# Performance work log

Measured on AMD Instinct MI355X. Metric: run time of the kernel, lower is better.

## Reference

```python
import jax, jax.numpy as jnp
import numpy as np
import math

NUM_HEADS = 8


def setup_inputs() -> dict:
    key = jax.random.key(0)
    ks = jax.random.split(key, 6)
    b, s, e = 4, 2048, 512
    x = jax.random.normal(ks[0], (b, s, e), dtype=jnp.float32)
    # 0/1 adjacency matrix as float (it multiplies the scores in the module)
    adj = jax.random.randint(ks[1], (b, s, s), 0, 2).astype(jnp.float32)
    scale = 0.02
    Wqkv_w = jax.random.normal(ks[2], (3 * e, e), dtype=jnp.float32) * scale
    Wqkv_b = jax.random.normal(ks[3], (3 * e,), dtype=jnp.float32) * scale
    out_w = jax.random.normal(ks[4], (e, e), dtype=jnp.float32) * scale
    out_b = jax.random.normal(ks[5], (e,), dtype=jnp.float32) * scale
    return {"x": x, "adj": adj, "Wqkv_w": Wqkv_w, "Wqkv_b": Wqkv_b,
            "out_w": out_w, "out_b": out_b}


def reference(x, adj, Wqkv_w, Wqkv_b, out_w, out_b):
    b, s, e = x.shape
    h = NUM_HEADS
    d = e // h
    # fused qkv projection: (b, s, 3*e) -> (b, s, 3, h, d)
    qkv = (x @ Wqkv_w.T + Wqkv_b).reshape(b, s, 3, h, d)
    qkv = jnp.transpose(qkv, (2, 0, 3, 1, 4))  # (3, b, h, s, d)
    q, k, v = qkv[0], qkv[1], qkv[2]
    inv_sqrt_d = 1.0 / math.sqrt(d)
    scores = jnp.einsum('bhqd,bhkd->bhqk', q, k) * inv_sqrt_d
    scores = jnp.clip(scores * adj[:, None, :, :], -10000.0, 10000.0)
    attn = jax.nn.softmax(scores, axis=-1)
    out = jnp.einsum('bhqk,bhkd->bhqd', attn, v)
    out = jnp.transpose(out, (0, 2, 1, 3)).reshape(b, s, e)  # (b, s, h*d)
    return out @ out_w.T + out_b
```

## Files before the change

kernel.cpp:

```cpp
#include <hip/hip_runtime.h>


typedef __attribute__((ext_vector_type(8))) short bf16x8;
typedef __attribute__((ext_vector_type(4))) float f32x4;
typedef __attribute__((ext_vector_type(4))) unsigned short ushort4v;
typedef __attribute__((ext_vector_type(4))) _Float16 f16x4;
typedef __attribute__((ext_vector_type(8))) _Float16 f16x8;
typedef __attribute__((ext_vector_type(2))) __fp16 h16x2;
typedef __attribute__((ext_vector_type(2))) unsigned long long u64x2;

#if __has_builtin(__builtin_amdgcn_exp2f)
#define EXP2F(x) __builtin_amdgcn_exp2f(x)
#else
#define EXP2F(x) exp2f(x)
#endif

#define QSCALE 0.18033688011112042f

__device__ __forceinline__ unsigned short f2bf(float f) {
  unsigned int u = __float_as_uint(f);
  u += 0x7FFFu + ((u >> 16) & 1u);
  return (unsigned short)(u >> 16);
}
__device__ __forceinline__ unsigned short f2h(float f) {
  union { _Float16 h; unsigned short u; } cv;
  cv.h = (_Float16)f;
  return cv.u;
}

__device__ __forceinline__ int sbit(unsigned w, int pos) {
  return ((int)(w << (31 - pos))) >> 31;
}

__device__ __forceinline__ f16x8 pk8(const float* p) {
  union { struct { h16x2 a, b, c, d; } s; f16x8 v; } u;
  u.s.a = __builtin_amdgcn_cvt_pkrtz(p[0], p[1]);
  u.s.b = __builtin_amdgcn_cvt_pkrtz(p[2], p[3]);
  u.s.c = __builtin_amdgcn_cvt_pkrtz(p[4], p[5]);
  u.s.d = __builtin_amdgcn_cvt_pkrtz(p[6], p[7]);
  return u.v;
}

__device__ __forceinline__ f32x4 mfma_pv(f16x8 a, f16x8 b, f32x4 c) {
#if __has_builtin(__builtin_amdgcn_mfma_f32_16x16x32_f16)
  return __builtin_amdgcn_mfma_f32_16x16x32_f16(a, b, c, 0, 0, 0);
#else
  union { f16x8 v; struct { f16x4 lo, hi; } s; } ua, ub;
  ua.v = a; ub.v = b;
  c = __builtin_amdgcn_mfma_f32_16x16x16f16(ua.s.lo, ub.s.lo, c, 0, 0, 0);
  return __builtin_amdgcn_mfma_f32_16x16x16f16(ua.s.hi, ub.s.hi, c, 0, 0, 0);
#endif
}

__global__ __launch_bounds__(256) void prep_k(const float* __restrict__ x,
                                              unsigned short* __restrict__ x_bf,
                                              const float* __restrict__ wqkv,
                                              unsigned short* __restrict__ wqkv_bf,
                                              const float* __restrict__ outw,
                                              unsigned short* __restrict__ outw_bf,
                                              const float* __restrict__ adj,
                                              unsigned long long* __restrict__ abits) {
  const int bid = blockIdx.x;
  if (bid < 5120) {
    const float* in; unsigned short* out; int i;
    if (bid < 4096) { in = x; out = x_bf; i = bid * 256 + threadIdx.x; }
    else if (bid < 4864) { in = wqkv; out = wqkv_bf; i = (bid - 4096) * 256 + threadIdx.x; }
    else { in = outw; out = outw_bf; i = (bid - 4864) * 256 + threadIdx.x; }
    float4 v = ((const float4*)in)[i];
    ushort4v o;
    o[0] = f2bf(v.x); o[1] = f2bf(v.y); o[2] = f2bf(v.z); o[3] = f2bf(v.w);
    ((ushort4v*)out)[i] = o;
  } else {
    const int gw = (bid - 5120) * 4 + (threadIdx.x >> 6);
    const int l = threadIdx.x & 63;
    const int b = gw >> 11, q = gw & 2047;
    const float4* row = (const float4*)(adj + ((size_t)b * 2048 + q) * 2048) + l;
    unsigned long long* ob = abits + ((size_t)b * 8 * 2048 + q) * 4;
#pragma unroll
    for (int it = 0; it < 8; ++it) {
      const float4 v = row[(size_t)it * 64];
      const unsigned long long w0 = __ballot(v.x != 0.f);
      const unsigned long long w1 = __ballot(v.y != 0.f);
      const unsigned long long w2 = __ballot(v.z != 0.f);
      const unsigned long long w3 = __ballot(v.w != 0.f);
      if (l == 0) {
        ob[(size_t)it * 8192 + 0] = w0;
        ob[(size_t)it * 8192 + 1] = w1;
        ob[(size_t)it * 8192 + 2] = w2;
        ob[(size_t)it * 8192 + 3] = w3;
      }
    }
  }
}

__global__ __launch_bounds__(256, 3) void gemm128_k(const unsigned short* __restrict__ A,
                                                    const unsigned short* __restrict__ Bt,
                                                    const float* __restrict__ bias, int Kdim,
                                                    int Ntiles, unsigned short* __restrict__ q_out,
                                                    unsigned short* __restrict__ k_out,
                                                    unsigned short* __restrict__ v_out) {
  __shared__ union {
    struct { unsigned short A[2][128][40], B[2][128][40]; } s;
    unsigned short T[64][136];
  } u;

  const int t = threadIdx.x;
  const int lane = t & 63, w = t >> 6, ln = lane & 15, quad = lane >> 4;
  const int xcd = blockIdx.x & 7, loc = blockIdx.x >> 3;
  const int mt = xcd * ((gridDim.x >> 3) / Ntiles) + loc / Ntiles;
  const int nt = loc % Ntiles;
  const int wm = (w >> 1) * 64, wn = (w & 1) * 64;
  const int strow = t >> 2, stcol = (t & 3) * 8;

  const size_t abase = (size_t)(mt * 128 + strow) * Kdim + stcol;
  const size_t bbase = (size_t)(nt * 128 + strow) * Kdim + stcol;

  f32x4 acc[4][4];
#pragma unroll
  for (int i = 0; i < 4; ++i)
#pragma unroll
    for (int j = 0; j < 4; ++j) acc[i][j] = (f32x4){0.f, 0.f, 0.f, 0.f};

  bf16x8 a0 = *(const bf16x8*)(A + abase);
  bf16x8 a1 = *(const bf16x8*)(A + abase + (size_t)64 * Kdim);
  bf16x8 b0 = *(const bf16x8*)(Bt + bbase);
  bf16x8 b1 = *(const bf16x8*)(Bt + bbase + (size_t)64 * Kdim);
  *(bf16x8*)&u.s.A[0][strow][stcol] = a0;
  *(bf16x8*)&u.s.A[0][64 + strow][stcol] = a1;
  *(bf16x8*)&u.s.B[0][strow][stcol] = b0;
  *(bf16x8*)&u.s.B[0][64 + strow][stcol] = b1;
  __syncthreads();

  const int iters = Kdim >> 5;
  for (int it = 0; it < iters; ++it) {
    const int cur = it & 1, nxt = cur ^ 1;

    const int kn = ((it + 1) << 5) & (Kdim - 1);
    a0 = *(const bf16x8*)(A + abase + kn);
    a1 = *(const bf16x8*)(A + abase + (size_t)64 * Kdim + kn);
    b0 = *(const bf16x8*)(Bt + bbase + kn);
    b1 = *(const bf16x8*)(Bt + bbase + (size_t)64 * Kdim + kn);

    bf16x8 bfr[4];
#pragma unroll
    for (int nf = 0; nf < 4; ++nf)
      bfr[nf] = *(const bf16x8*)&u.s.B[cur][wn + nf * 16 + ln][quad * 8];
#pragma unroll
    for (int mf = 0; mf < 4; ++mf) {
      bf16x8 af = *(const bf16x8*)&u.s.A[cur][wm + mf * 16 + ln][quad * 8];
#pragma unroll
      for (int nf = 0; nf < 4; ++nf)
        acc[mf][nf] = __builtin_amdgcn_mfma_f32_16x16x32_bf16(af, bfr[nf], acc[mf][nf], 0, 0, 0);
    }

    if (it + 1 < iters) {
      *(bf16x8*)&u.s.A[nxt][strow][stcol] = a0;
      *(bf16x8*)&u.s.A[nxt][64 + strow][stcol] = a1;
      *(bf16x8*)&u.s.B[nxt][strow][stcol] = b0;
      *(bf16x8*)&u.s.B[nxt][64 + strow][stcol] = b1;
      __syncthreads();
    }
  }

  if (nt >= 8) {
    const int bb = mt >> 4, sq0 = (mt & 15) * 128;
#pragma unroll
    for (int half = 0; half < 2; ++half) {
      __syncthreads();
      if ((w & 1) == half) {
#pragma unroll
        for (int nf = 0; nf < 4; ++nf) {
          const float bv = bias[nt * 128 + half * 64 + nf * 16 + ln];
#pragma unroll
          for (int mf = 0; mf < 4; ++mf)
#pragma unroll
            for (int r = 0; r < 4; ++r)
              u.T[nf * 16 + ln][wm + mf * 16 + quad * 4 + r] = f2h(acc[mf][nf][r] + bv);
        }
      }
      __syncthreads();
#pragma unroll
      for (int rep = 0; rep < 4; ++rep) {
        const int row = rep * 16 + (t >> 4), c = t & 15;
        const bf16x8 val = *(const bf16x8*)&u.T[row][c * 8];
        const int hd = (nt - 8) * 128 + half * 64 + row;
        const int hh = hd >> 6, dd = hd & 63;
        *(bf16x8*)(v_out + ((size_t)(bb * 8 + hh) * 64 + dd) * 2048 + sq0 + c * 8) = val;
      }
    }
    return;
  }

#pragma unroll
  for (int mf = 0; mf < 4; ++mf) {
    const int m = mt * 128 + wm + mf * 16 + quad * 4;
#pragma unroll
    for (int nf = 0; nf < 4; ++nf) {
      const int n = nt * 128 + wn + nf * 16 + ln;
      const float bv = bias[n];
      const int hd = n & 511;
      const int hh = hd >> 6, dd = hd & 63;
      const int bb = m >> 11, sq = m & 2047;
      if (n < 512) {
#pragma unroll
        for (int r = 0; r < 4; ++r)
          q_out[((size_t)(bb * 8 + hh) * 2048 + sq + r) * 64 + dd] =
              f2bf((acc[mf][nf][r] + bv) * QSCALE);
      } else {
#pragma unroll
        for (int r = 0; r < 4; ++r)
          k_out[((size_t)(bb * 8 + hh) * 2048 + sq + r) * 64 + dd] = f2bf(acc[mf][nf][r] + bv);
      }
    }
  }
}

__global__ __launch_bounds__(256, 4) void gemm64_k(const unsigned short* __restrict__ A,
                                                   const unsigned short* __restrict__ Bt,
                                                   const float* __restrict__ bias,
                                                   float* __restrict__ f_out) {
  __shared__ struct { unsigned short A[2][64][40], B[2][64][40]; } s;

  const int t = threadIdx.x;
  const int lane = t & 63, w = t >> 6, ln = lane & 15, quad = lane >> 4;
  const int xcd = blockIdx.x & 7, loc = blockIdx.x >> 3;
  const int mt = xcd * 16 + (loc >> 3);
  const int nt = loc & 7;
  const int wm = (w >> 1) * 32, wn = (w & 1) * 32;
  const int strow = t >> 2, stcol = (t & 3) * 8;

  const size_t abase = (size_t)(mt * 64 + strow) * 512 + stcol;
  const size_t bbase = (size_t)(nt * 64 + strow) * 512 + stcol;

  f32x4 acc[2][2];
#pragma unroll
  for (int i = 0; i < 2; ++i)
#pragma unroll
    for (int j = 0; j < 2; ++j) acc[i][j] = (f32x4){0.f, 0.f, 0.f, 0.f};

  bf16x8 a0 = *(const bf16x8*)(A + abase);
  bf16x8 b0 = *(const bf16x8*)(Bt + bbase);
  *(bf16x8*)&s.A[0][strow][stcol] = a0;
  *(bf16x8*)&s.B[0][strow][stcol] = b0;
  __syncthreads();

  for (int it = 0; it < 16; ++it) {
    const int cur = it & 1, nxt = cur ^ 1;

    const int kn = ((it + 1) << 5) & 511;
    a0 = *(const bf16x8*)(A + abase + kn);
    b0 = *(const bf16x8*)(Bt + bbase + kn);

    bf16x8 bfr[2];
#pragma unroll
    for (int nf = 0; nf < 2; ++nf)
      bfr[nf] = *(const bf16x8*)&s.B[cur][wn + nf * 16 + ln][quad * 8];
#pragma unroll
    for (int mf = 0; mf < 2; ++mf) {
      bf16x8 af = *(const bf16x8*)&s.A[cur][wm + mf * 16 + ln][quad * 8];
#pragma unroll
      for (int nf = 0; nf < 2; ++nf)
        acc[mf][nf] = __builtin_amdgcn_mfma_f32_16x16x32_bf16(af, bfr[nf], acc[mf][nf], 0, 0, 0);
    }

    if (it + 1 < 16) {
      *(bf16x8*)&s.A[nxt][strow][stcol] = a0;
      *(bf16x8*)&s.B[nxt][strow][stcol] = b0;
      __syncthreads();
    }
  }

#pragma unroll
  for (int mf = 0; mf < 2; ++mf) {
    const int m = mt * 64 + wm + mf * 16 + quad * 4;
#pragma unroll
    for (int nf = 0; nf < 2; ++nf) {
      const int n = nt * 64 + wn + nf * 16 + ln;
      const float bv = bias[n];
#pragma unroll
      for (int r = 0; r < 4; ++r) f_out[(size_t)(m + r) * 512 + n] = acc[mf][nf][r] + bv;
    }
  }
}

__global__ __launch_bounds__(256, 2) void attn_k(const unsigned short* __restrict__ Qg,
                                                 const unsigned short* __restrict__ Kg,
                                                 const unsigned short* __restrict__ Vg,
                                                 const unsigned long long* __restrict__ Mg,
                                                 unsigned short* __restrict__ Og) {
  __shared__ unsigned short K_lds[2][64][64];
  __shared__ unsigned short V_lds[2][64][64];

  const int t = threadIdx.x;
  const int w = t >> 6, lane = t & 63, ln = lane & 15, quad = lane >> 4;
  const int bh = blockIdx.x & 31, qt = blockIdx.x >> 5, bb = bh >> 3;
  const int sbase = qt * 128;

  const unsigned short* Qp = Qg + (size_t)bh * (2048 * 64);
  const unsigned short* Kp = Kg + (size_t)bh * (2048 * 64);
  const unsigned short* Vp = Vg + (size_t)bh * (64 * 2048);
  const unsigned long long* Mb = Mg + ((size_t)bb * 8 * 2048 + sbase + w * 32 + ln) * 4;

  bf16x8 qf[2][2];
#pragma unroll
  for (int qg = 0; qg < 2; ++qg) {
    const int qrow = sbase + w * 32 + qg * 16 + ln;
    qf[qg][0] = *(const bf16x8*)(Qp + (size_t)qrow * 64 + quad * 8);
    qf[qg][1] = *(const bf16x8*)(Qp + (size_t)qrow * 64 + 32 + quad * 8);
  }

  const _Float16 one_h = (_Float16)((ln == 0) ? 1.0f : 0.0f);
  const f16x8 vf_one = (f16x8){one_h, one_h, one_h, one_h, one_h, one_h, one_h, one_h};

  const f32x4 zf = (f32x4){0.f, 0.f, 0.f, 0.f};

  f32x4 acc_o[2][4];
#pragma unroll
  for (int qg = 0; qg < 2; ++qg)
#pragma unroll
    for (int dg = 0; dg < 4; ++dg) acc_o[qg][dg] = zf;
  f32x4 acc_1[2] = {zf, zf};

  const int strow = t >> 2;
  const int stcol = (t & 3) * 16;
  const int c0 = (t & 3) * 2;
  const int gkw = (strow & 3) | (((strow >> 3) & 1) << 2);
  const int gvw = strow & 7;

  const unsigned short* Kl = Kp + (size_t)strow * 64 + stcol;
  const unsigned short* Vl = Vp + (size_t)strow * 2048 + stcol;

  bf16x8 kr0 = *(const bf16x8*)(Kl);
  bf16x8 kr1 = *(const bf16x8*)(Kl + 8);
  bf16x8 vr0 = *(const bf16x8*)(Vl);
  bf16x8 vr1 = *(const bf16x8*)(Vl + 8);
  *(bf16x8*)&K_lds[0][strow][(c0 ^ gkw) << 3] = kr0;
  *(bf16x8*)&K_lds[0][strow][((c0 + 1) ^ gkw) << 3] = kr1;
  *(bf16x8*)&V_lds[0][strow][(c0 ^ gvw) << 3] = vr0;
  *(bf16x8*)&V_lds[0][strow][((c0 + 1) ^ gvw) << 3] = vr1;
  u64x2 Wlo[2], Whi[2];
#pragma unroll
  for (int qg = 0; qg < 2; ++qg) {
    Wlo[qg] = *(const u64x2*)(Mb + qg * 64);
    Whi[qg] = *(const u64x2*)(Mb + qg * 64 + 2);
  }
  __syncthreads();

  const int kperm = ((ln >> 2) << 3) + (ln & 3);
  const int gkr = (ln & 3) | (((ln >> 2) & 1) << 2);
  const int gvr = ln & 7;
  const int kc = (quad ^ gkr) << 3;
  const unsigned q2 = quad << 1;

  for (int kts = 0; kts < 8; ++kts) {
    const size_t itn = (size_t)((kts < 7) ? kts + 1 : 0) * 8192;
    u64x2 nWlo[2], nWhi[2];
#pragma unroll
    for (int qg = 0; qg < 2; ++qg) {
      nWlo[qg] = *(const u64x2*)(Mb + itn + qg * 64);
      nWhi[qg] = *(const u64x2*)(Mb + itn + qg * 64 + 2);
    }

#pragma unroll
    for (int j = 0; j < 4; ++j) {
      const int kt = kts * 4 + j;
      const int cur = j & 1, nxt = cur ^ 1;

      kr0 = *(const bf16x8*)(Kl + (size_t)(kt + 1) * 4096);
      kr1 = *(const bf16x8*)(Kl + (size_t)(kt + 1) * 4096 + 8);
      vr0 = *(const bf16x8*)(Vl + (kt + 1) * 64);
      vr1 = *(const bf16x8*)(Vl + (kt + 1) * 64 + 8);

      f32x4 sc[2][4];
      __builtin_amdgcn_s_setprio(1);
#pragma unroll
      for (int h = 0; h < 2; ++h)
#pragma unroll
        for (int e = 0; e < 2; ++e) {
          const int krow = h * 32 + kperm + e * 4;
          bf16x8 kf0 = *(const bf16x8*)&K_lds[cur][krow][kc];
          bf16x8 kf1 = *(const bf16x8*)&K_lds[cur][krow][kc ^ 32];
#pragma unroll
          for (int qg = 0; qg < 2; ++qg) {
            f32x4 z = __builtin_amdgcn_mfma_f32_16x16x32_bf16(kf0, qf[qg][0], zf, 0, 0, 0);
            sc[qg][h * 2 + e] = __builtin_amdgcn_mfma_f32_16x16x32_bf16(kf1, qf[qg][1], z, 0, 0, 0);
          }
        }
      __builtin_amdgcn_s_setprio(0);

      f16x8 vfa[2][4];
#pragma unroll
      for (int h = 0; h < 2; ++h)
#pragma unroll
        for (int dg = 0; dg < 4; ++dg)
          vfa[h][dg] = *(const f16x8*)&V_lds[cur][dg * 16 + ln][((h * 4 + quad) ^ gvr) << 3];

      f16x8 pa[2][2];
#pragma unroll
      for (int qg = 0; qg < 2; ++qg) {
        const unsigned s0 = (unsigned)(Wlo[qg][0] >> (j >= 2 ? 32 : 0)) >> q2;
        const unsigned s1 = (unsigned)(Wlo[qg][1] >> (j >= 2 ? 32 : 0)) >> q2;
        const unsigned s2 = (unsigned)(Whi[qg][0] >> (j >= 2 ? 32 : 0)) >> q2;
        const unsigned s3 = (unsigned)(Whi[qg][1] >> (j >= 2 ? 32 : 0)) >> q2;
#pragma unroll
        for (int h = 0; h < 2; ++h) {
          float p[8];
#pragma unroll
          for (int e = 0; e < 2; ++e) {
            const int pos = (j & 1) * 16 + h * 8 + e;
            p[e * 4 + 0] =
                EXP2F(__int_as_float(__float_as_int(sc[qg][h * 2 + e][0]) & sbit(s0, pos)));
            p[e * 4 + 1] =
                EXP2F(__int_as_float(__float_as_int(sc[qg][h * 2 + e][1]) & sbit(s1, pos)));
            p[e * 4 + 2] =
                EXP2F(__int_as_float(__float_as_int(sc[qg][h * 2 + e][2]) & sbit(s2, pos)));
            p[e * 4 + 3] =
                EXP2F(__int_as_float(__float_as_int(sc[qg][h * 2 + e][3]) & sbit(s3, pos)));
          }
          pa[qg][h] = pk8(p);
        }
      }

      __builtin_amdgcn_s_setprio(1);
#pragma unroll
      for (int h = 0; h < 2; ++h)
#pragma unroll
        for (int qg = 0; qg < 2; ++qg) {
#pragma unroll
          for (int dg = 0; dg < 4; ++dg)
            acc_o[qg][dg] = mfma_pv(pa[qg][h], vfa[h][dg], acc_o[qg][dg]);
          acc_1[qg] = mfma_pv(pa[qg][h], vf_one, acc_1[qg]);
        }
      __builtin_amdgcn_s_setprio(0);

      if (kt < 31) {
        *(bf16x8*)&K_lds[nxt][strow][(c0 ^ gkw) << 3] = kr0;
        *(bf16x8*)&K_lds[nxt][strow][((c0 + 1) ^ gkw) << 3] = kr1;
        *(bf16x8*)&V_lds[nxt][strow][(c0 ^ gvw) << 3] = vr0;
        *(bf16x8*)&V_lds[nxt][strow][((c0 + 1) ^ gvw) << 3] = vr1;
        __syncthreads();
      }
    }
    Wlo[0] = nWlo[0]; Wlo[1] = nWlo[1];
    Whi[0] = nWhi[0]; Whi[1] = nWhi[1];
  }

  unsigned short* Op = Og + (size_t)bb * 2048 * 512 + (size_t)(bh & 7) * 64;
#pragma unroll
  for (int qg = 0; qg < 2; ++qg)
#pragma unroll
    for (int r = 0; r < 4; ++r) {
      const float inv = 1.0f / __shfl(acc_1[qg][r], quad * 16);
      const int sq = sbase + w * 32 + qg * 16 + quad * 4 + r;
#pragma unroll
      for (int dg = 0; dg < 4; ++dg)
        Op[(size_t)sq * 512 + dg * 16 + ln] = f2bf(acc_o[qg][dg][r] * inv);
    }
}

extern "C" void kernel_launch(void* const* d_in, const int* in_sizes, int n_in, void* d_out,
                              int out_size, void* d_ws, size_t ws_size, hipStream_t stream) {
  const float* x = (const float*)d_in[0];
  const float* adj = (const float*)d_in[1];
  const float* wqkv = (const float*)d_in[2];
  const float* bqkv = (const float*)d_in[3];
  const float* outw = (const float*)d_in[4];
  const float* outb = (const float*)d_in[5];
  float* out = (float*)d_out;

  char* ws = (char*)d_ws;
  unsigned short* x_bf = (unsigned short*)(ws);
  unsigned short* wqkv_bf = (unsigned short*)(ws + 8388608);
  unsigned short* outw_bf = (unsigned short*)(ws + 9961472);
  unsigned long long* abits = (unsigned long long*)(ws + 10485760);
  unsigned short* Qb = (unsigned short*)(ws + 27262976);
  unsigned short* Kb = (unsigned short*)(ws + 35651584);
  unsigned short* Vb = (unsigned short*)(ws + 44040192);
  unsigned short* Ob = (unsigned short*)(ws + 52428800);

  prep_k<<<7168, 256, 0, stream>>>(x, x_bf, wqkv, wqkv_bf, outw, outw_bf, adj, abits);

  gemm128_k<<<768, 256, 0, stream>>>(x_bf, wqkv_bf, bqkv, 512, 12, Qb, Kb, Vb);

  attn_k<<<512, 256, 0, stream>>>(Qb, Kb, Vb, abits, Ob);

  gemm64_k<<<1024, 256, 0, stream>>>(Ob, outw_bf, outb, out);
}
```

Before: 200.6 us.

## Fuse all stages into one persistent kernel with grid barriers

Merges the prep, QKV GEMM, attention and output GEMM kernels into a single persistent launch of 512 blocks that loops over the former block indices, with atomic-counter grid barriers between stages and a shared-memory union. The aim is to remove kernel launch gaps and tail effects between stages. In exchange it adds a memset launch and spin-wait barriers. Correctness depends on all 512 blocks being co-resident. It also forces a single occupancy setting (launch_bounds 256,2) on every stage, which may lower occupancy for the GEMMs that previously ran with 3 or 4 blocks per unit.

After: 507.1 us. 153% more time.

```diff
diff --git a/kernel.cpp b/kernel.cpp
--- a/kernel.cpp
+++ b/kernel.cpp
@@ -52,410 +52,426 @@
 #endif
 }
 
-__global__ __launch_bounds__(256) void prep_k(const float* __restrict__ x,
-                                              unsigned short* __restrict__ x_bf,
-                                              const float* __restrict__ wqkv,
-                                              unsigned short* __restrict__ wqkv_bf,
-                                              const float* __restrict__ outw,
-                                              unsigned short* __restrict__ outw_bf,
-                                              const float* __restrict__ adj,
-                                              unsigned long long* __restrict__ abits) {
-  const int bid = blockIdx.x;
-  if (bid < 5120) {
-    const float* in; unsigned short* out; int i;
-    if (bid < 4096) { in = x; out = x_bf; i = bid * 256 + threadIdx.x; }
-    else if (bid < 4864) { in = wqkv; out = wqkv_bf; i = (bid - 4096) * 256 + threadIdx.x; }
-    else { in = outw; out = outw_bf; i = (bid - 4864) * 256 + threadIdx.x; }
-    float4 v = ((const float4*)in)[i];
-    ushort4v o;
-    o[0] = f2bf(v.x); o[1] = f2bf(v.y); o[2] = f2bf(v.z); o[3] = f2bf(v.w);
-    ((ushort4v*)out)[i] = o;
-  } else {
-    const int gw = (bid - 5120) * 4 + (threadIdx.x >> 6);
-    const int l = threadIdx.x & 63;
-    const int b = gw >> 11, q = gw & 2047;
-    const float4* row = (const float4*)(adj + ((size_t)b * 2048 + q) * 2048) + l;
-    unsigned long long* ob = abits + ((size_t)b * 8 * 2048 + q) * 4;
-#pragma unroll
-    for (int it = 0; it < 8; ++it) {
-      const float4 v = row[(size_t)it * 64];
-      const unsigned long long w0 = __ballot(v.x != 0.f);
-      const unsigned long long w1 = __ballot(v.y != 0.f);
-      const unsigned long long w2 = __ballot(v.z != 0.f);
-      const unsigned long long w3 = __ballot(v.w != 0.f);
-      if (l == 0) {
-        ob[(size_t)it * 8192 + 0] = w0;
-        ob[(size_t)it * 8192 + 1] = w1;
-        ob[(size_t)it * 8192 + 2] = w2;
-        ob[(size_t)it * 8192 + 3] = w3;
-      }
-    }
-  }
-}
-
-__global__ __launch_bounds__(256, 3) void gemm128_k(const unsigned short* __restrict__ A,
-                                                    const unsigned short* __restrict__ Bt,
-                                                    const float* __restrict__ bias, int Kdim,
-                                                    int Ntiles, unsigned short* __restrict__ q_out,
-                                                    unsigned short* __restrict__ k_out,
-                                                    unsigned short* __restrict__ v_out) {
-  __shared__ union {
-    struct { unsigned short A[2][128][40], B[2][128][40]; } s;
-    unsigned short T[64][136];
-  } u;
-
-  const int t = threadIdx.x;
-  const int lane = t & 63, w = t >> 6, ln = lane & 15, quad = lane >> 4;
-  const int xcd = blockIdx.x & 7, loc = blockIdx.x >> 3;
-  const int mt = xcd * ((gridDim.x >> 3) / Ntiles) + loc / Ntiles;
-  const int nt = loc % Ntiles;
-  const int wm = (w >> 1) * 64, wn = (w & 1) * 64;
-  const int strow = t >> 2, stcol = (t & 3) * 8;
-
-  const size_t abase = (size_t)(mt * 128 + strow) * Kdim + stcol;
-  const size_t bbase = (size_t)(nt * 128 + strow) * Kdim + stcol;
-
-  f32x4 acc[4][4];
-#pragma unroll
-  for (int i = 0; i < 4; ++i)
-#pragma unroll
-    for (int j = 0; j < 4; ++j) acc[i][j] = (f32x4){0.f, 0.f, 0.f, 0.f};
-
-  bf16x8 a0 = *(const bf16x8*)(A + abase);
-  bf16x8 a1 = *(const bf16x8*)(A + abase + (size_t)64 * Kdim);
-  bf16x8 b0 = *(const bf16x8*)(Bt + bbase);
-  bf16x8 b1 = *(const bf16x8*)(Bt + bbase + (size_t)64 * Kdim);
-  *(bf16x8*)&u.s.A[0][strow][stcol] = a0;
-  *(bf16x8*)&u.s.A[0][64 + strow][stcol] = a1;
-  *(bf16x8*)&u.s.B[0][strow][stcol] = b0;
-  *(bf16x8*)&u.s.B[0][64 + strow][stcol] = b1;
+__device__ __forceinline__ void gridbar(unsigned* c) {
   __syncthreads();
-
-  const int iters = Kdim >> 5;
-  for (int it = 0; it < iters; ++it) {
-    const int cur = it & 1, nxt = cur ^ 1;
-
-    const int kn = ((it + 1) << 5) & (Kdim - 1);
-    a0 = *(const bf16x8*)(A + abase + kn);
-    a1 = *(const bf16x8*)(A + abase + (size_t)64 * Kdim + kn);
-    b0 = *(const bf16x8*)(Bt + bbase + kn);
-    b1 = *(const bf16x8*)(Bt + bbase + (size_t)64 * Kdim + kn);
-
-    bf16x8 bfr[4];
-#pragma unroll
-    for (int nf = 0; nf < 4; ++nf)
-      bfr[nf] = *(const bf16x8*)&u.s.B[cur][wn + nf * 16 + ln][quad * 8];
-#pragma unroll
-    for (int mf = 0; mf < 4; ++mf) {
-      bf16x8 af = *(const bf16x8*)&u.s.A[cur][wm + mf * 16 + ln][quad * 8];
-#pragma unroll
-      for (int nf = 0; nf < 4; ++nf)
-        acc[mf][nf] = __builtin_amdgcn_mfma_f32_16x16x32_bf16(af, bfr[nf], acc[mf][nf], 0, 0, 0);
-    }
-
-    if (it + 1 < iters) {
-      *(bf16x8*)&u.s.A[nxt][strow][stcol] = a0;
-      *(bf16x8*)&u.s.A[nxt][64 + strow][stcol] = a1;
-      *(bf16x8*)&u.s.B[nxt][strow][stcol] = b0;
-      *(bf16x8*)&u.s.B[nxt][64 + strow][stcol] = b1;
-      __syncthreads();
-    }
-  }
-
-  if (nt >= 8) {
-    const int bb = mt >> 4, sq0 = (mt & 15) * 128;
-#pragma unroll
-    for (int half = 0; half < 2; ++half) {
-      __syncthreads();
-      if ((w & 1) == half) {
-#pragma unroll
-        for (int nf = 0; nf < 4; ++nf) {
-          const float bv = bias[nt * 128 + half * 64 + nf * 16 + ln];
-#pragma unroll
-          for (int mf = 0; mf < 4; ++mf)
-#pragma unroll
-            for (int r = 0; r < 4; ++r)
-              u.T[nf * 16 + ln][wm + mf * 16 + quad * 4 + r] = f2h(acc[mf][nf][r] + bv);
-        }
-      }
-      __syncthreads();
-#pragma unroll
-      for (int rep = 0; rep < 4; ++rep) {
-        const int row = rep * 16 + (t >> 4), c = t & 15;
-        const bf16x8 val = *(const bf16x8*)&u.T[row][c * 8];
-        const int hd = (nt - 8) * 128 + half * 64 + row;
-        const int hh = hd >> 6, dd = hd & 63;
-        *(bf16x8*)(v_out + ((size_t)(bb * 8 + hh) * 64 + dd) * 2048 + sq0 + c * 8) = val;
-      }
-    }
-    return;
-  }
-
-#pragma unroll
-  for (int mf = 0; mf < 4; ++mf) {
-    const int m = mt * 128 + wm + mf * 16 + quad * 4;
-#pragma unroll
-    for (int nf = 0; nf < 4; ++nf) {
-      const int n = nt * 128 + wn + nf * 16 + ln;
-      const float bv = bias[n];
-      const int hd = n & 511;
-      const int hh = hd >> 6, dd = hd & 63;
-      const int bb = m >> 11, sq = m & 2047;
-      if (n < 512) {
-#pragma unroll
-        for (int r = 0; r < 4; ++r)
-          q_out[((size_t)(bb * 8 + hh) * 2048 + sq + r) * 64 + dd] =
-              f2bf((acc[mf][nf][r] + bv) * QSCALE);
-      } else {
-#pragma unroll
-        for (int r = 0; r < 4; ++r)
-          k_out[((size_t)(bb * 8 + hh) * 2048 + sq + r) * 64 + dd] = f2bf(acc[mf][nf][r] + bv);
-      }
-    }
-  }
-}
-
-__global__ __launch_bounds__(256, 4) void gemm64_k(const unsigned short* __restrict__ A,
-                                                   const unsigned short* __restrict__ Bt,
-                                                   const float* __restrict__ bias,
-                                                   float* __restrict__ f_out) {
-  __shared__ struct { unsigned short A[2][64][40], B[2][64][40]; } s;
-
-  const int t = threadIdx.x;
-  const int lane = t & 63, w = t >> 6, ln = lane & 15, quad = lane >> 4;
-  const int xcd = blockIdx.x & 7, loc = blockIdx.x >> 3;
-  const int mt = xcd * 16 + (loc >> 3);
-  const int nt = loc & 7;
-  const int wm = (w >> 1) * 32, wn = (w & 1) * 32;
-  const int strow = t >> 2, stcol = (t & 3) * 8;
-
-  const size_t abase = (size_t)(mt * 64 + strow) * 512 + stcol;
-  const size_t bbase = (size_t)(nt * 64 + strow) * 512 + stcol;
-
-  f32x4 acc[2][2];
-#pragma unroll
-  for (int i = 0; i < 2; ++i)
-#pragma unroll
-    for (int j = 0; j < 2; ++j) acc[i][j] = (f32x4){0.f, 0.f, 0.f, 0.f};
-
-  bf16x8 a0 = *(const bf16x8*)(A + abase);
-  bf16x8 b0 = *(const bf16x8*)(Bt + bbase);
-  *(bf16x8*)&s.A[0][strow][stcol] = a0;
-  *(bf16x8*)&s.B[0][strow][stcol] = b0;
-  __syncthreads();
-
-  for (int it = 0; it < 16; ++it) {
-    const int cur = it & 1, nxt = cur ^ 1;
-
-    const int kn = ((it + 1) << 5) & 511;
-    a0 = *(const bf16x8*)(A + abase + kn);
-    b0 = *(const bf16x8*)(Bt + bbase + kn);
-
-    bf16x8 bfr[2];
-#pragma unroll
-    for (int nf = 0; nf < 2; ++nf)
-      bfr[nf] = *(const bf16x8*)&s.B[cur][wn + nf * 16 + ln][quad * 8];
-#pragma unroll
-    for (int mf = 0; mf < 2; ++mf) {
-      bf16x8 af = *(const bf16x8*)&s.A[cur][wm + mf * 16 + ln][quad * 8];
-#pragma unroll
-      for (int nf = 0; nf < 2; ++nf)
-        acc[mf][nf] = __builtin_amdgcn_mfma_f32_16x16x32_bf16(af, bfr[nf], acc[mf][nf], 0, 0, 0);
-    }
-
-    if (it + 1 < 16) {
-      *(bf16x8*)&s.A[nxt][strow][stcol] = a0;
-      *(bf16x8*)&s.B[nxt][strow][stcol] = b0;
-      __syncthreads();
-    }
-  }
-
-#pragma unroll
-  for (int mf = 0; mf < 2; ++mf) {
-    const int m = mt * 64 + wm + mf * 16 + quad * 4;
-#pragma unroll
-    for (int nf = 0; nf < 2; ++nf) {
-      const int n = nt * 64 + wn + nf * 16 + ln;
-      const float bv = bias[n];
-#pragma unroll
-      for (int r = 0; r < 4; ++r) f_out[(size_t)(m + r) * 512 + n] = acc[mf][nf][r] + bv;
-    }
-  }
-}
-
-__global__ __launch_bounds__(256, 2) void attn_k(const unsigned short* __restrict__ Qg,
-                                                 const unsigned short* __restrict__ Kg,
-                                                 const unsigned short* __restrict__ Vg,
-                                                 const unsigned long long* __restrict__ Mg,
-                                                 unsigned short* __restrict__ Og) {
-  __shared__ unsigned short K_lds[2][64][64];
-  __shared__ unsigned short V_lds[2][64][64];
-
-  const int t = threadIdx.x;
-  const int w = t >> 6, lane = t & 63, ln = lane & 15, quad = lane >> 4;
-  const int bh = blockIdx.x & 31, qt = blockIdx.x >> 5, bb = bh >> 3;
-  const int sbase = qt * 128;
-
-  const unsigned short* Qp = Qg + (size_t)bh * (2048 * 64);
-  const unsigned short* Kp = Kg + (size_t)bh * (2048 * 64);
-  const unsigned short* Vp = Vg + (size_t)bh * (64 * 2048);
-  const unsigned long long* Mb = Mg + ((size_t)bb * 8 * 2048 + sbase + w * 32 + ln) * 4;
-
-  bf16x8 qf[2][2];
-#pragma unroll
-  for (int qg = 0; qg < 2; ++qg) {
-    const int qrow = sbase + w * 32 + qg * 16 + ln;
-    qf[qg][0] = *(const bf16x8*)(Qp + (size_t)qrow * 64 + quad * 8);
-    qf[qg][1] = *(const bf16x8*)(Qp + (size_t)qrow * 64 + 32 + quad * 8);
-  }
-
-  const _Float16 one_h = (_Float16)((ln == 0) ? 1.0f : 0.0f);
-  const f16x8 vf_one = (f16x8){one_h, one_h, one_h, one_h, one_h, one_h, one_h, one_h};
-
-  const f32x4 zf = (f32x4){0.f, 0.f, 0.f, 0.f};
-
-  f32x4 acc_o[2][4];
-#pragma unroll
-  for (int qg = 0; qg < 2; ++qg)
-#pragma unroll
-    for (int dg = 0; dg < 4; ++dg) acc_o[qg][dg] = zf;
-  f32x4 acc_1[2] = {zf, zf};
-
-  const int strow = t >> 2;
-  const int stcol = (t & 3) * 16;
-  const int c0 = (t & 3) * 2;
-  const int gkw = (strow & 3) | (((strow >> 3) & 1) << 2);
-  const int gvw = strow & 7;
-
-  const unsigned short* Kl = Kp + (size_t)strow * 64 + stcol;
-  const unsigned short* Vl = Vp + (size_t)strow * 2048 + stcol;
-
-  bf16x8 kr0 = *(const bf16x8*)(Kl);
-  bf16x8 kr1 = *(const bf16x8*)(Kl + 8);
-  bf16x8 vr0 = *(const bf16x8*)(Vl);
-  bf16x8 vr1 = *(const bf16x8*)(Vl + 8);
-  *(bf16x8*)&K_lds[0][strow][(c0 ^ gkw) << 3] = kr0;
-  *(bf16x8*)&K_lds[0][strow][((c0 + 1) ^ gkw) << 3] = kr1;
-  *(bf16x8*)&V_lds[0][strow][(c0 ^ gvw) << 3] = vr0;
-  *(bf16x8*)&V_lds[0][strow][((c0 + 1) ^ gvw) << 3] = vr1;
-  u64x2 Wlo[2], Whi[2];
-#pragma unroll
-  for (int qg = 0; qg < 2; ++qg) {
-    Wlo[qg] = *(const u64x2*)(Mb + qg * 64);
-    Whi[qg] = *(const u64x2*)(Mb + qg * 64 + 2);
+  if (threadIdx.x == 0) {
+    __threadfence();
+    __hip_atomic_fetch_add(c, 1u, __ATOMIC_RELEASE, __HIP_MEMORY_SCOPE_AGENT);
+    while (__hip_atomic_load(c, __ATOMIC_ACQUIRE, __HIP_MEMORY_SCOPE_AGENT) < 512u)
+      __builtin_amdgcn_s_sleep(8);
+    __threadfence();
   }
   __syncthreads();
-
-  const int kperm = ((ln >> 2) << 3) + (ln & 3);
-  const int gkr = (ln & 3) | (((ln >> 2) & 1) << 2);
-  const int gvr = ln & 7;
-  const int kc = (quad ^ gkr) << 3;
-  const unsigned q2 = quad << 1;
-
-  for (int kts = 0; kts < 8; ++kts) {
-    const size_t itn = (size_t)((kts < 7) ? kts + 1 : 0) * 8192;
-    u64x2 nWlo[2], nWhi[2];
-#pragma unroll
-    for (int qg = 0; qg < 2; ++qg) {
-      nWlo[qg] = *(const u64x2*)(Mb + itn + qg * 64);
-      nWhi[qg] = *(const u64x2*)(Mb + itn + qg * 64 + 2);
-    }
-
-#pragma unroll
-    for (int j = 0; j < 4; ++j) {
-      const int kt = kts * 4 + j;
-      const int cur = j & 1, nxt = cur ^ 1;
-
-      kr0 = *(const bf16x8*)(Kl + (size_t)(kt + 1) * 4096);
-      kr1 = *(const bf16x8*)(Kl + (size_t)(kt + 1) * 4096 + 8);
-      vr0 = *(const bf16x8*)(Vl + (kt + 1) * 64);
-      vr1 = *(const bf16x8*)(Vl + (kt + 1) * 64 + 8);
-
-      f32x4 sc[2][4];
-      __builtin_amdgcn_s_setprio(1);
-#pragma unroll
-      for (int h = 0; h < 2; ++h)
-#pragma unroll
-        for (int e = 0; e < 2; ++e) {
-          const int krow = h * 32 + kperm + e * 4;
-          bf16x8 kf0 = *(const bf16x8*)&K_lds[cur][krow][kc];
-          bf16x8 kf1 = *(const bf16x8*)&K_lds[cur][krow][kc ^ 32];
-#pragma unroll
-          for (int qg = 0; qg < 2; ++qg) {
-            f32x4 z = __builtin_amdgcn_mfma_f32_16x16x32_bf16(kf0, qf[qg][0], zf, 0, 0, 0);
-            sc[qg][h * 2 + e] = __builtin_amdgcn_mfma_f32_16x16x32_bf16(kf1, qf[qg][1], z, 0, 0, 0);
+}
+
+union ShMem {
+  struct { unsigned short A[2][128][40], B[2][128][40]; } g0;
+  unsigned short T[64][136];
+  struct { unsigned short K[2][64][64], V[2][64][64]; } at;
+  struct { unsigned short A[2][64][40], B[2][64][40]; } g1;
+};
+
+__global__ __launch_bounds__(256, 2) void fused_all(
+    const float* x, unsigned short* x_bf, const float* wqkv, unsigned short* wqkv_bf,
+    const float* outw, unsigned short* outw_bf, const float* adj,
+    unsigned long long* abits, const float* bqkv, unsigned short* Qb,
+    unsigned short* Kb, unsigned short* Vb, unsigned short* Ob,
+    const float* outb, float* out, unsigned* ctr) {
+  __shared__ ShMem sh;
+
+  const int t = threadIdx.x;
+  const int blk = blockIdx.x;
+  const int lane = t & 63, w = t >> 6, ln = lane & 15, quad = lane >> 4;
+
+#pragma unroll 1
+  for (int i = 0; i < 14; ++i) {
+    const int bid = blk + i * 512;
+    if (bid < 5120) {
+      const float* in; unsigned short* outp; int idx;
+      if (bid < 4096) { in = x; outp = x_bf; idx = bid * 256 + t; }
+      else if (bid < 4864) { in = wqkv; outp = wqkv_bf; idx = (bid - 4096) * 256 + t; }
+      else { in = outw; outp = outw_bf; idx = (bid - 4864) * 256 + t; }
+      float4 v = ((const float4*)in)[idx];
+      ushort4v o;
+      o[0] = f2bf(v.x); o[1] = f2bf(v.y); o[2] = f2bf(v.z); o[3] = f2bf(v.w);
+      ((ushort4v*)outp)[idx] = o;
+    } else {
+      const int gw = (bid - 5120) * 4 + (t >> 6);
+      const int l = t & 63;
+      const int b = gw >> 11, q = gw & 2047;
+      const float4* row = (const float4*)(adj + ((size_t)b * 2048 + q) * 2048) + l;
+      unsigned long long* ob = abits + ((size_t)b * 8 * 2048 + q) * 4;
+#pragma unroll
+      for (int it = 0; it < 8; ++it) {
+        const float4 v = row[(size_t)it * 64];
+        const unsigned long long w0 = __ballot(v.x != 0.f);
+        const unsigned long long w1 = __ballot(v.y != 0.f);
+        const unsigned long long w2 = __ballot(v.z != 0.f);
+        const unsigned long long w3 = __ballot(v.w != 0.f);
+        if (l == 0) {
+          ob[(size_t)it * 8192 + 0] = w0;
+          ob[(size_t)it * 8192 + 1] = w1;
+          ob[(size_t)it * 8192 + 2] = w2;
+          ob[(size_t)it * 8192 + 3] = w3;
+        }
+      }
+    }
+  }
+
+  gridbar(ctr + 0);
+
+#pragma unroll 1
+  for (int rep = 0; rep < 2; ++rep) {
+    const int bid = blk + rep * 512;
+    if (bid >= 768) break;
+    __syncthreads();
+
+    const int Ntiles = 12, Kdim = 512;
+    const int xcd = bid & 7, loc = bid >> 3;
+    const int mt = xcd * 8 + loc / Ntiles;
+    const int nt = loc % Ntiles;
+    const int wm = (w >> 1) * 64, wn = (w & 1) * 64;
+    const int strow = t >> 2, stcol = (t & 3) * 8;
+
+    const unsigned short* A = x_bf;
+    const unsigned short* Bt = wqkv_bf;
+
+    const size_t abase = (size_t)(mt * 128 + strow) * Kdim + stcol;
+    const size_t bbase = (size_t)(nt * 128 + strow) * Kdim + stcol;
+
+    f32x4 acc[4][4];
+#pragma unroll
+    for (int i = 0; i < 4; ++i)
+#pragma unroll
+      for (int j = 0; j < 4; ++j) acc[i][j] = (f32x4){0.f, 0.f, 0.f, 0.f};
+
+    bf16x8 a0 = *(const bf16x8*)(A + abase);
+    bf16x8 a1 = *(const bf16x8*)(A + abase + (size_t)64 * Kdim);
+    bf16x8 b0 = *(const bf16x8*)(Bt + bbase);
+    bf16x8 b1 = *(const bf16x8*)(Bt + bbase + (size_t)64 * Kdim);
+    *(bf16x8*)&sh.g0.A[0][strow][stcol] = a0;
+    *(bf16x8*)&sh.g0.A[0][64 + strow][stcol] = a1;
+    *(bf16x8*)&sh.g0.B[0][strow][stcol] = b0;
+    *(bf16x8*)&sh.g0.B[0][64 + strow][stcol] = b1;
+    __syncthreads();
+
+    for (int it = 0; it < 16; ++it) {
+      const int cur = it & 1, nxt = cur ^ 1;
+
+      const int kn = ((it + 1) << 5) & (Kdim - 1);
+      a0 = *(const bf16x8*)(A + abase + kn);
+      a1 = *(const bf16x8*)(A + abase + (size_t)64 * Kdim + kn);
+      b0 = *(const bf16x8*)(Bt + bbase + kn);
+      b1 = *(const bf16x8*)(Bt + bbase + (size_t)64 * Kdim + kn);
+
+      bf16x8 bfr[4];
+#pragma unroll
+      for (int nf = 0; nf < 4; ++nf)
+        bfr[nf] = *(const bf16x8*)&sh.g0.B[cur][wn + nf * 16 + ln][quad * 8];
+#pragma unroll
+      for (int mf = 0; mf < 4; ++mf) {
+        bf16x8 af = *(const bf16x8*)&sh.g0.A[cur][wm + mf * 16 + ln][quad * 8];
+#pragma unroll
+        for (int nf = 0; nf < 4; ++nf)
+          acc[mf][nf] = __builtin_amdgcn_mfma_f32_16x16x32_bf16(af, bfr[nf], acc[mf][nf], 0, 0, 0);
+      }
+
+      if (it + 1 < 16) {
+        *(bf16x8*)&sh.g0.A[nxt][strow][stcol] = a0;
+        *(bf16x8*)&sh.g0.A[nxt][64 + strow][stcol] = a1;
+        *(bf16x8*)&sh.g0.B[nxt][strow][stcol] = b0;
+        *(bf16x8*)&sh.g0.B[nxt][64 + strow][stcol] = b1;
+        __syncthreads();
+      }
+    }
+
+    if (nt >= 8) {
+      const int bb = mt >> 4, sq0 = (mt & 15) * 128;
+#pragma unroll
+      for (int half = 0; half < 2; ++half) {
+        __syncthreads();
+        if ((w & 1) == half) {
+#pragma unroll
+          for (int nf = 0; nf < 4; ++nf) {
+            const float bv = bqkv[nt * 128 + half * 64 + nf * 16 + ln];
+#pragma unroll
+            for (int mf = 0; mf < 4; ++mf)
+#pragma unroll
+              for (int r = 0; r < 4; ++r)
+                sh.T[nf * 16 + ln][wm + mf * 16 + quad * 4 + r] = f2h(acc[mf][nf][r] + bv);
           }
         }
-      __builtin_amdgcn_s_setprio(0);
-
-      f16x8 vfa[2][4];
-#pragma unroll
-      for (int h = 0; h < 2; ++h)
+        __syncthreads();
+#pragma unroll
+        for (int rep2 = 0; rep2 < 4; ++rep2) {
+          const int row = rep2 * 16 + (t >> 4), c = t & 15;
+          const bf16x8 val = *(const bf16x8*)&sh.T[row][c * 8];
+          const int hd = (nt - 8) * 128 + half * 64 + row;
+          const int hh = hd >> 6, dd = hd & 63;
+          *(bf16x8*)(Vb + ((size_t)(bb * 8 + hh) * 64 + dd) * 2048 + sq0 + c * 8) = val;
+        }
+      }
+    } else {
+#pragma unroll
+      for (int mf = 0; mf < 4; ++mf) {
+        const int m = mt * 128 + wm + mf * 16 + quad * 4;
+#pragma unroll
+        for (int nf = 0; nf < 4; ++nf) {
+          const int n = nt * 128 + wn + nf * 16 + ln;
+          const float bv = bqkv[n];
+          const int hd = n & 511;
+          const int hh = hd >> 6, dd = hd & 63;
+          const int bb = m >> 11, sq = m & 2047;
+          if (n < 512) {
+#pragma unroll
+            for (int r = 0; r < 4; ++r)
+              Qb[((size_t)(bb * 8 + hh) * 2048 + sq + r) * 64 + dd] =
+                  f2bf((acc[mf][nf][r] + bv) * QSCALE);
+          } else {
+#pragma unroll
+            for (int r = 0; r < 4; ++r)
+              Kb[((size_t)(bb * 8 + hh) * 2048 + sq + r) * 64 + dd] = f2bf(acc[mf][nf][r] + bv);
+          }
+        }
+      }
+    }
+  }
+
+  gridbar(ctr + 1);
+
+  {
+    const int bh = blk & 31, qt = blk >> 5, bb = bh >> 3;
+    const int sbase = qt * 128;
+
+    const unsigned short* Qp = Qb + (size_t)bh * (2048 * 64);
+    const unsigned short* Kp = Kb + (size_t)bh * (2048 * 64);
+    const unsigned short* Vp = Vb + (size_t)bh * (64 * 2048);
+    const unsigned long long* Mb = abits + ((size_t)bb * 8 * 2048 + sbase + w * 32 + ln) * 4;
+
+    bf16x8 qf[2][2];
+#pragma unroll
+    for (int qg = 0; qg < 2; ++qg) {
+      const int qrow = sbase + w * 32 + qg * 16 + ln;
+      qf[qg][0] = *(const bf16x8*)(Qp + (size_t)qrow * 64 + quad * 8);
+      qf[qg][1] = *(const bf16x8*)(Qp + (size_t)qrow * 64 + 32 + quad * 8);
+    }
+
+    const _Float16 one_h = (_Float16)((ln == 0) ? 1.0f : 0.0f);
+    const f16x8 vf_one = (f16x8){one_h, one_h, one_h, one_h, one_h, one_h, one_h, one_h};
+
+    const f32x4 zf = (f32x4){0.f, 0.f, 0.f, 0.f};
+
+    f32x4 acc_o[2][4];
+#pragma unroll
+    for (int qg = 0; qg < 2; ++qg)
+#pragma unroll
+      for (int dg = 0; dg < 4; ++dg) acc_o[qg][dg] = zf;
+    f32x4 acc_1[2] = {zf, zf};
+
+    const int strow = t >> 2;
+    const int stcol = (t & 3) * 16;
+    const int c0 = (t & 3) * 2;
+    const int gkw = (strow & 3) | (((strow >> 3) & 1) << 2);
+    const int gvw = strow & 7;
+
+    const unsigned short* Kl = Kp + (size_t)strow * 64 + stcol;
+    const unsigned short* Vl = Vp + (size_t)strow * 2048 + stcol;
+
+    bf16x8 kr0 = *(const bf16x8*)(Kl);
+    bf16x8 kr1 = *(const bf16x8*)(Kl + 8);
+    bf16x8 vr0 = *(const bf16x8*)(Vl);
+    bf16x8 vr1 = *(const bf16x8*)(Vl + 8);
+    *(bf16x8*)&sh.at.K[0][strow][(c0 ^ gkw) << 3] = kr0;
+    *(bf16x8*)&sh.at.K[0][strow][((c0 + 1) ^ gkw) << 3] = kr1;
+    *(bf16x8*)&sh.at.V[0][strow][(c0 ^ gvw) << 3] = vr0;
+    *(bf16x8*)&sh.at.V[0][strow][((c0 + 1) ^ gvw) << 3] = vr1;
+    u64x2 Wlo[2], Whi[2];
+#pragma unroll
+    for (int qg = 0; qg < 2; ++qg) {
+      Wlo[qg] = *(const u64x2*)(Mb + qg * 64);
+      Whi[qg] = *(const u64x2*)(Mb + qg * 64 + 2);
+    }
+    __syncthreads();
+
+    const int kperm = ((ln >> 2) << 3) + (ln & 3);
+    const int gkr = (ln & 3) | (((ln >> 2) & 1) << 2);
+    const int gvr = ln & 7;
+    const int kc = (quad ^ gkr) << 3;
+    const unsigned q2 = quad << 1;
+
+    for (int kts = 0; kts < 8; ++kts) {
+      const size_t itn = (size_t)((kts < 7) ? kts + 1 : 0) * 8192;
+      u64x2 nWlo[2], nWhi[2];
+#pragma unroll
+      for (int qg = 0; qg < 2; ++qg) {
+        nWlo[qg] = *(const u64x2*)(Mb + itn + qg * 64);
+        nWhi[qg] = *(const u64x2*)(Mb + itn + qg * 64 + 2);
+      }
+
+#pragma unroll
+      for (int j = 0; j < 4; ++j) {
+        const int kt = kts * 4 + j;
+        const int cur = j & 1, nxt = cur ^ 1;
+
+        kr0 = *(const bf16x8*)(Kl + (size_t)(kt + 1) * 4096);
+        kr1 = *(const bf16x8*)(Kl + (size_t)(kt + 1) * 4096 + 8);
+        vr0 = *(const bf16x8*)(Vl + (kt + 1) * 64);
+        vr1 = *(const bf16x8*)(Vl + (kt + 1) * 64 + 8);
+
+        f32x4 sc[2][4];
+        __builtin_amdgcn_s_setprio(1);
+#pragma unroll
+        for (int h = 0; h < 2; ++h)
+#pragma unroll
+          for (int e = 0; e < 2; ++e) {
+            const int krow = h * 32 + kperm + e * 4;
+            bf16x8 kf0 = *(const bf16x8*)&sh.at.K[cur][krow][kc];
+            bf16x8 kf1 = *(const bf16x8*)&sh.at.K[cur][krow][kc ^ 32];
+#pragma unroll
+            for (int qg = 0; qg < 2; ++qg) {
+              f32x4 z = __builtin_amdgcn_mfma_f32_16x16x32_bf16(kf0, qf[qg][0], zf, 0, 0, 0);
+              sc[qg][h * 2 + e] =
+                  __builtin_amdgcn_mfma_f32_16x16x32_bf16(kf1, qf[qg][1], z, 0, 0, 0);
+            }
+          }
+        __builtin_amdgcn_s_setprio(0);
+
+        f16x8 vfa[2][4];
+#pragma unroll
+        for (int h = 0; h < 2; ++h)
+#pragma unroll
+          for (int dg = 0; dg < 4; ++dg)
+            vfa[h][dg] = *(const f16x8*)&sh.at.V[cur][dg * 16 + ln][((h * 4 + quad) ^ gvr) << 3];
+
+        f16x8 pa[2][2];
+#pragma unroll
+        for (int qg = 0; qg < 2; ++qg) {
+          const unsigned s0 = (unsigned)(Wlo[qg][0] >> (j >= 2 ? 32 : 0)) >> q2;
+          const unsigned s1 = (unsigned)(Wlo[qg][1] >> (j >= 2 ? 32 : 0)) >> q2;
+          const unsigned s2 = (unsigned)(Whi[qg][0] >> (j >= 2 ? 32 : 0)) >> q2;
+          const unsigned s3 = (unsigned)(Whi[qg][1] >> (j >= 2 ? 32 : 0)) >> q2;
+#pragma unroll
+          for (int h = 0; h < 2; ++h) {
+            float p[8];
+#pragma unroll
+            for (int e = 0; e < 2; ++e) {
+              const int pos = (j & 1) * 16 + h * 8 + e;
+              p[e * 4 + 0] =
+                  EXP2F(__int_as_float(__float_as_int(sc[qg][h * 2 + e][0]) & sbit(s0, pos)));
+              p[e * 4 + 1] =
+                  EXP2F(__int_as_float(__float_as_int(sc[qg][h * 2 + e][1]) & sbit(s1, pos)));
+              p[e * 4 + 2] =
+                  EXP2F(__int_as_float(__float_as_int(sc[qg][h * 2 + e][2]) & sbit(s2, pos)));
+              p[e * 4 + 3] =
+                  EXP2F(__int_as_float(__float_as_int(sc[qg][h * 2 + e][3]) & sbit(s3, pos)));
+            }
+            pa[qg][h] = pk8(p);
+          }
+        }
+
+        __builtin_amdgcn_s_setprio(1);
+#pragma unroll
+        for (int h = 0; h < 2; ++h)
+#pragma unroll
+          for (int qg = 0; qg < 2; ++qg) {
+#pragma unroll
+            for (int dg = 0; dg < 4; ++dg)
+              acc_o[qg][dg] = mfma_pv(pa[qg][h], vfa[h][dg], acc_o[qg][dg]);
+            acc_1[qg] = mfma_pv(pa[qg][h], vf_one, acc_1[qg]);
+          }
+        __builtin_amdgcn_s_setprio(0);
+
+        if (kt < 31) {
+          *(bf16x8*)&sh.at.K[nxt][strow][(c0 ^ gkw) << 3] = kr0;
+          *(bf16x8*)&sh.at.K[nxt][strow][((c0 + 1) ^ gkw) << 3] = kr1;
+          *(bf16x8*)&sh.at.V[nxt][strow][(c0 ^ gvw) << 3] = vr0;
+          *(bf16x8*)&sh.at.V[nxt][strow][((c0 + 1) ^ gvw) << 3] = vr1;
+          __syncthreads();
+        }
+      }
+      Wlo[0] = nWlo[0]; Wlo[1] = nWlo[1];
+      Whi[0] = nWhi[0]; Whi[1] = nWhi[1];
+    }
+
+    unsigned short* Op = Ob + (size_t)bb * 2048 * 512 + (size_t)(bh & 7) * 64;
+#pragma unroll
+    for (int qg = 0; qg < 2; ++qg)
+#pragma unroll
+      for (int r = 0; r < 4; ++r) {
+        const float inv = 1.0f / __shfl(acc_1[qg][r], quad * 16);
+        const int sq = sbase + w * 32 + qg * 16 + quad * 4 + r;
 #pragma unroll
         for (int dg = 0; dg < 4; ++dg)
-          vfa[h][dg] = *(const f16x8*)&V_lds[cur][dg * 16 + ln][((h * 4 + quad) ^ gvr) << 3];
-
-      f16x8 pa[2][2];
-#pragma unroll
-      for (int qg = 0; qg < 2; ++qg) {
-        const unsigned s0 = (unsigned)(Wlo[qg][0] >> (j >= 2 ? 32 : 0)) >> q2;
-        const unsigned s1 = (unsigned)(Wlo[qg][1] >> (j >= 2 ? 32 : 0)) >> q2;
-        const unsigned s2 = (unsigned)(Whi[qg][0] >> (j >= 2 ? 32 : 0)) >> q2;
-        const unsigned s3 = (unsigned)(Whi[qg][1] >> (j >= 2 ? 32 : 0)) >> q2;
-#pragma unroll
-        for (int h = 0; h < 2; ++h) {
-          float p[8];
-#pragma unroll
-          for (int e = 0; e < 2; ++e) {
-            const int pos = (j & 1) * 16 + h * 8 + e;
-            p[e * 4 + 0] =
-                EXP2F(__int_as_float(__float_as_int(sc[qg][h * 2 + e][0]) & sbit(s0, pos)));
-            p[e * 4 + 1] =
-                EXP2F(__int_as_float(__float_as_int(sc[qg][h * 2 + e][1]) & sbit(s1, pos)));
-            p[e * 4 + 2] =
-                EXP2F(__int_as_float(__float_as_int(sc[qg][h * 2 + e][2]) & sbit(s2, pos)));
-            p[e * 4 + 3] =
-                EXP2F(__int_as_float(__float_as_int(sc[qg][h * 2 + e][3]) & sbit(s3, pos)));
-          }
-          pa[qg][h] = pk8(p);
-        }
-      }
-
-      __builtin_amdgcn_s_setprio(1);
-#pragma unroll
-      for (int h = 0; h < 2; ++h)
-#pragma unroll
-        for (int qg = 0; qg < 2; ++qg) {
-#pragma unroll
-          for (int dg = 0; dg < 4; ++dg)
-            acc_o[qg][dg] = mfma_pv(pa[qg][h], vfa[h][dg], acc_o[qg][dg]);
-          acc_1[qg] = mfma_pv(pa[qg][h], vf_one, acc_1[qg]);
-        }
-      __builtin_amdgcn_s_setprio(0);
-
-      if (kt < 31) {
-        *(bf16x8*)&K_lds[nxt][strow][(c0 ^ gkw) << 3] = kr0;
-        *(bf16x8*)&K_lds[nxt][strow][((c0 + 1) ^ gkw) << 3] = kr1;
-        *(bf16x8*)&V_lds[nxt][strow][(c0 ^ gvw) << 3] = vr0;
-        *(bf16x8*)&V_lds[nxt][strow][((c0 + 1) ^ gvw) << 3] = vr1;
+          Op[(size_t)sq * 512 + dg * 16 + ln] = f2bf(acc_o[qg][dg][r] * inv);
+      }
+  }
+
+  gridbar(ctr + 2);
+
+#pragma unroll 1
+  for (int rep = 0; rep < 2; ++rep) {
+    const int bid = blk + rep * 512;
+    __syncthreads();
+
+    const int xcd = bid & 7, loc = bid >> 3;
+    const int mt = xcd * 16 + (loc >> 3);
+    const int nt = loc & 7;
+    const int wm = (w >> 1) * 32, wn = (w & 1) * 32;
+    const int strow = t >> 2, stcol = (t & 3) * 8;
+
+    const size_t abase = (size_t)(mt * 64 + strow) * 512 + stcol;
+    const size_t bbase = (size_t)(nt * 64 + strow) * 512 + stcol;
+
+    f32x4 acc[2][2];
+#pragma unroll
+    for (int i = 0; i < 2; ++i)
+#pragma unroll
+      for (int j = 0; j < 2; ++j) acc[i][j] = (f32x4){0.f, 0.f, 0.f, 0.f};
+
+    bf16x8 a0 = *(const bf16x8*)(Ob + abase);
+    bf16x8 b0 = *(const bf16x8*)(outw_bf + bbase);
+    *(bf16x8*)&sh.g1.A[0][strow][stcol] = a0;
+    *(bf16x8*)&sh.g1.B[0][strow][stcol] = b0;
+    __syncthreads();
+
+    for (int it = 0; it < 16; ++it) {
+      const int cur = it & 1, nxt = cur ^ 1;
+
+      const int kn = ((it + 1) << 5) & 511;
+      a0 = *(const bf16x8*)(Ob + abase + kn);
+      b0 = *(const bf16x8*)(outw_bf + bbase + kn);
+
+      bf16x8 bfr[2];
+#pragma unroll
+      for (int nf = 0; nf < 2; ++nf)
+        bfr[nf] = *(const bf16x8*)&sh.g1.B[cur][wn + nf * 16 + ln][quad * 8];
+#pragma unroll
+      for (int mf = 0; mf < 2; ++mf) {
+        bf16x8 af = *(const bf16x8*)&sh.g1.A[cur][wm + mf * 16 + ln][quad * 8];
+#pragma unroll
+        for (int nf = 0; nf < 2; ++nf)
+          acc[mf][nf] = __builtin_amdgcn_mfma_f32_16x16x32_bf16(af, bfr[nf], acc[mf][nf], 0, 0, 0);
+      }
+
+      if (it + 1 < 16) {
+        *(bf16x8*)&sh.g1.A[nxt][strow][stcol] = a0;
+        *(bf16x8*)&sh.g1.B[nxt][strow][stcol] = b0;
         __syncthreads();
       }
     }
-    Wlo[0] = nWlo[0]; Wlo[1] = nWlo[1];
-    Whi[0] = nWhi[0]; Whi[1] = nWhi[1];
+
+#pragma unroll
+    for (int mf = 0; mf < 2; ++mf) {
+      const int m = mt * 64 + wm + mf * 16 + quad * 4;
+#pragma unroll
+      for (int nf = 0; nf < 2; ++nf) {
+        const int n = nt * 64 + wn + nf * 16 + ln;
+        const float bv = outb[n];
+#pragma unroll
+        for (int r = 0; r < 4; ++r) out[(size_t)(m + r) * 512 + n] = acc[mf][nf][r] + bv;
+      }
+    }
   }
-
-  unsigned short* Op = Og + (size_t)bb * 2048 * 512 + (size_t)(bh & 7) * 64;
-#pragma unroll
-  for (int qg = 0; qg < 2; ++qg)
-#pragma unroll
-    for (int r = 0; r < 4; ++r) {
-      const float inv = 1.0f / __shfl(acc_1[qg][r], quad * 16);
-      const int sq = sbase + w * 32 + qg * 16 + quad * 4 + r;
-#pragma unroll
-      for (int dg = 0; dg < 4; ++dg)
-        Op[(size_t)sq * 512 + dg * 16 + ln] = f2bf(acc_o[qg][dg][r] * inv);
-    }
 }
 
 extern "C" void kernel_launch(void* const* d_in, const int* in_sizes, int n_in, void* d_out,
@@ -473,16 +489,14 @@
   unsigned short* wqkv_bf = (unsigned short*)(ws + 8388608);
   unsigned short* outw_bf = (unsigned short*)(ws + 9961472);
   unsigned long long* abits = (unsigned long long*)(ws + 10485760);
+  unsigned* ctr = (unsigned*)(ws + 25165824);
   unsigned short* Qb = (unsigned short*)(ws + 27262976);
   unsigned short* Kb = (unsigned short*)(ws + 35651584);
   unsigned short* Vb = (unsigned short*)(ws + 44040192);
   unsigned short* Ob = (unsigned short*)(ws + 52428800);
 
-  prep_k<<<7168, 256, 0, stream>>>(x, x_bf, wqkv, wqkv_bf, outw, outw_bf, adj, abits);
-
-  gemm128_k<<<768, 256, 0, stream>>>(x_bf, wqkv_bf, bqkv, 512, 12, Qb, Kb, Vb);
-
-  attn_k<<<512, 256, 0, stream>>>(Qb, Kb, Vb, abits, Ob);
-
-  gemm64_k<<<1024, 256, 0, stream>>>(Ob, outw_bf, outb, out);
-}
+  hipMemsetAsync(ctr, 0, 64, stream);
+
+  fused_all<<<512, 256, 0, stream>>>(x, x_bf, wqkv, wqkv_bf, outw, outw_bf, adj, abits,
+                                     bqkv, Qb, Kb, Vb, Ob, outb, out, ctr);
+}
```
